# Kernel optimization log

Hardware: AMD Instinct MI355X
Metric: run time of the kernel (lower is better)

The kernel has to match this reference:

```python
import jax, jax.numpy as jnp
import numpy as np

N = 100000

def _gcn_layer(x, W, b, row, col, n):
    # x: [N, Fin] -> lin -> [N, Fout]
    h = x @ W + b
    # degree over row (includes self loops), dtype follows x
    deg = jnp.zeros((n,), dtype=h.dtype).at[row].add(jnp.ones_like(row, dtype=h.dtype))
    dis = deg ** -0.5
    norm = dis[row] * dis[col]                      # [E]
    msg = norm[:, None] * h[row]                    # gather + scale: [E, Fout]
    return jax.ops.segment_sum(msg, col, num_segments=n)  # scatter-add at targets


def setup_inputs() -> dict:
    key = jax.random.key(0)
    ks = jax.random.split(key, 10)
    x = jax.random.normal(ks[0], (N, 32), dtype=jnp.float32)
    feat = jax.random.normal(ks[1], (N, 32), dtype=jnp.float32)
    edge_index = jax.random.randint(ks[2], (2, 1600000), 0, N, dtype=jnp.int64)
    # params (torch Linear stored as [in, out] here; y = x @ W + b)
    def lin(k, fin, fout):
        s = 1.0 / np.sqrt(fin)
        kw, kb = jax.random.split(k)
        W = jax.random.uniform(kw, (fin, fout), minval=-s, maxval=s, dtype=jnp.float32)
        b = jax.random.uniform(kb, (fout,), minval=-s, maxval=s, dtype=jnp.float32)
        return W, b
    W1, b1 = lin(ks[3], 64, 64)
    W2, b2 = lin(ks[4], 64, 64)
    Wfc, bfc = lin(ks[5], 64, 64)
    return {"x": x, "feat": feat, "edge_index": edge_index,
            "W1": W1, "b1": b1, "W2": W2, "b2": b2, "Wfc": Wfc, "bfc": bfc}


def reference(x, feat, edge_index, W1, b1, W2, b2, Wfc, bfc):
    n = x.shape[0]
    h = jnp.concatenate([x, feat], axis=-1)          # [N, 64]
    # add self loops once (same augmented edge set used by every layer)
    loops = jnp.arange(n, dtype=edge_index.dtype)
    row = jnp.concatenate([edge_index[0], loops])
    col = jnp.concatenate([edge_index[1], loops])
    h = jax.nn.relu(_gcn_layer(h, W1, b1, row, col, n))
    h = jax.nn.relu(_gcn_layer(h, W2, b2, row, col, n))
    return jax.nn.relu(h @ Wfc + bfc)                # [N, 64]
```

## Files before the change

kernel.cpp:

```cpp
#include <hip/hip_runtime.h>
#include <hip/hip_bf16.h>


#define FDIM 64
#define NPART 8
#define GPB 64
#define NB 256
#define BW 512
#define MAXP 1024
#define GPLIN 1024

typedef __hip_bfloat16 bf16;
typedef short v8s __attribute__((ext_vector_type(8)));
typedef float v4f __attribute__((ext_vector_type(4)));

static __device__ __forceinline__ float ulo2f(unsigned u) {
    union { unsigned x; float f; } v; v.x = u << 16; return v.f;
}
static __device__ __forceinline__ float uhi2f(unsigned u) {
    union { unsigned x; float f; } v; v.x = u & 0xFFFF0000u; return v.f;
}
static __device__ __forceinline__ unsigned f2bu(float f) {
    bf16 b = __float2bfloat16(f);
    return (unsigned)(*(unsigned short*)&b);
}

__global__ void k_h(const int* __restrict__ row, const int* __restrict__ col,
                    unsigned* __restrict__ part, int* __restrict__ M,
                    int E, int n, int psize, int P, int CH) {
    __shared__ unsigned sm[12512];
    int t = threadIdx.x, b = blockIdx.x;
    if (b < NPART * GPB) {
        int p = b >> 6, g = b & 63;
        int base = p * psize;
        int lim = n - base; if (lim > psize) lim = psize;
        for (int i = t; i < lim; i += 256) sm[i] = 0u;
        __syncthreads();
        for (int e = g * 256 + t; e < E; e += GPB * 256) {
            int r = row[e] - base;
            if ((unsigned)r < (unsigned)lim) atomicAdd(&sm[r], 1u);
        }
        __syncthreads();
        unsigned* dst = part + ((size_t)p * GPB + g) * psize;
        for (int i = t; i < lim; i += 256) dst[i] = sm[i];
    } else {
        int cb = b - NPART * GPB;
        int* h = (int*)sm;
        for (int i = t; i < P; i += 256) h[i] = 0;
        __syncthreads();
        int s = cb * CH, e = min(s + CH, E);
        for (int i = s + t; i < e; i += 256)
            atomicAdd(&h[col[i] >> 9], 1);
        __syncthreads();
        for (int p = t; p < P; p += 256) M[p * NB + cb] = h[p];
    }
}

__global__ void k_ds1(const unsigned* __restrict__ part, float* __restrict__ dis,
                      int* __restrict__ M, int* __restrict__ bsum,
                      int n, int psize, int ndis, int P) {
    __shared__ int sc[256];
    int t = threadIdx.x, b = blockIdx.x;
    if (b < ndis) {
        int i = b * 256 + t;
        if (i >= n) return;
        int p = i / psize, loc = i - p * psize;
        const unsigned* src = part + (size_t)p * GPB * psize + loc;
        unsigned s = 0;
        #pragma unroll 8
        for (int g = 0; g < GPB; ++g) s += src[(size_t)g * psize];
        dis[i] = rsqrtf((float)s + 1.0f);
    } else {
        int sb = b - ndis;
        int i = sb * 256 + t;
        int v = M[i];
        sc[t] = v;
        __syncthreads();
        for (int d = 1; d < 256; d <<= 1) {
            int u = (t >= d) ? sc[t - d] : 0;
            __syncthreads(); sc[t] += u; __syncthreads();
        }
        M[i] = sc[t] - v;
        if (t == 255) bsum[sb] = sc[255];
    }
}

__global__ void k_csc(const int* __restrict__ row, const int* __restrict__ col,
                      const int* __restrict__ M, const int* __restrict__ bsum,
                      int* __restrict__ s4, int E, int CH, int P) {
    __shared__ int sc[256];
    __shared__ int bs[256];
    __shared__ int cur[MAXP];
    int t = threadIdx.x, b = blockIdx.x;
    int v = (t < P) ? bsum[t] : 0;
    sc[t] = v;
    __syncthreads();
    for (int d = 1; d < 256; d <<= 1) {
        int u = (t >= d) ? sc[t - d] : 0;
        __syncthreads(); sc[t] += u; __syncthreads();
    }
    bs[t] = sc[t] - v;
    __syncthreads();
    for (int p = t; p < P; p += 256) cur[p] = bs[p] + M[p * NB + b];
    __syncthreads();
    int s = b * CH, e = min(s + CH, E);
    for (int i = s + t; i < e; i += 256) {
        int r = row[i], c = col[i];
        int pos = atomicAdd(&cur[c >> 9], 1);
        s4[pos] = (r << 9) | (c & 511);
    }
}

__global__ __launch_bounds__(256, 4)
void k_fl(const int* __restrict__ s4, const int* __restrict__ M,
          const int* __restrict__ bsum, int* __restrict__ rows4,
          int* __restrict__ off,
          const float* __restrict__ x, const float* __restrict__ feat,
          const float* __restrict__ W, const float* __restrict__ bvec,
          const float* __restrict__ dis, bf16* __restrict__ g1,
          int n, int E, int P) {
    __shared__ int sc[256];
    __shared__ int bs[256];
    __shared__ int hist[BW];
    __shared__ int loff[BW];
    __shared__ int tmp[256];
    __shared__ float sIn[4][FDIM];
    int t = threadIdx.x, b = blockIdx.x;
    if (b < P) {
        int v = (t < P) ? bsum[t] : 0;
        sc[t] = v;
        __syncthreads();
        for (int d = 1; d < 256; d <<= 1) {
            int u = (t >= d) ? sc[t - d] : 0;
            __syncthreads(); sc[t] += u; __syncthreads();
        }
        bs[t] = sc[t] - v;
        __syncthreads();
        int gs = bs[b];
        int ge = gs + bsum[b];
        int c0 = b << 9;
        int lim = n - c0; if (lim > BW) lim = BW;
        hist[2 * t] = 0; hist[2 * t + 1] = 0;
        __syncthreads();
        for (int i = gs + t; i < ge; i += 256)
            atomicAdd(&hist[s4[i] & 511], 1);
        __syncthreads();
        int s0 = hist[2 * t], s1v = hist[2 * t + 1];
        int ps = s0 + s1v;
        tmp[t] = ps;
        __syncthreads();
        for (int d = 1; d < 256; d <<= 1) {
            int u = (t >= d) ? tmp[t - d] : 0;
            __syncthreads(); tmp[t] += u; __syncthreads();
        }
        int ex = tmp[t] - ps;
        loff[2 * t] = ex;
        loff[2 * t + 1] = ex + s0;
        __syncthreads();
        for (int i = t; i < lim; i += 256) off[c0 + i] = gs + loff[i];
        if (b == P - 1 && t == 0) off[n] = E;
        __syncthreads();
        for (int i = gs + t; i < ge; i += 256) {
            int v2 = s4[i];
            int pos = gs + atomicAdd(&loff[v2 & 511], 1);
            rows4[pos] = v2 >> 9;
        }
    } else {
        int local = t >> 6, j = t & 63;
        float Wreg[FDIM];
        #pragma unroll
        for (int k = 0; k < FDIM; ++k) Wreg[k] = W[k * FDIM + j];
        float bj = bvec[j];
        int gw = (b - P) * 4 + local;
        int nwl = GPLIN * 4;
        for (int w = gw; w < n; w += nwl) {
            sIn[local][j] = (j < 32) ? x[(size_t)w * 32 + j]
                                     : feat[(size_t)w * 32 + (j - 32)];
            __threadfence_block();
            float o = bj;
            #pragma unroll
            for (int k4 = 0; k4 < 16; ++k4) {
                float4 h4 = *(const float4*)&sIn[local][k4 * 4];
                o = fmaf(h4.x, Wreg[4 * k4 + 0], o);
                o = fmaf(h4.y, Wreg[4 * k4 + 1], o);
                o = fmaf(h4.z, Wreg[4 * k4 + 2], o);
                o = fmaf(h4.w, Wreg[4 * k4 + 3], o);
            }
            g1[(size_t)w * FDIM + j] = __float2bfloat16(dis[w] * o);
            __threadfence_block();
        }
    }
}

__global__ __launch_bounds__(256, 8)
void k_gather(const int* __restrict__ rows4, const int* __restrict__ off,
              const float* __restrict__ dis, const bf16* __restrict__ g,
              bf16* __restrict__ a, int n) {
    int t = blockIdx.x * blockDim.x + threadIdx.x;
    int w = t >> 6;
    if (w >= n) return;
    int lane = threadIdx.x & 63;
    int h = lane >> 5;
    int j2 = lane & 31;
    const unsigned* g32 = (const unsigned*)g;
    float acc0 = 0.0f, acc1 = 0.0f;
    int s = off[w], e = off[w + 1];
    for (int k = s; k < e; k += 16) {
        #pragma unroll
        for (int i = 0; i < 8; ++i) {
            int idx = k + 2 * i + h;
            int r = rows4[min(idx, e - 1)];
            unsigned u = g32[(size_t)r * 32 + j2];
            float wg = (idx < e) ? 1.0f : 0.0f;
            acc0 = fmaf(wg, ulo2f(u), acc0);
            acc1 = fmaf(wg, uhi2f(u), acc1);
        }
    }
    acc0 += __shfl_xor(acc0, 32, 64);
    acc1 += __shfl_xor(acc1, 32, 64);
    if (h == 0) {
        unsigned su = g32[(size_t)w * 32 + j2];
        float dv = dis[w];
        float v0 = fmaxf(dv * (acc0 + ulo2f(su)), 0.0f);
        float v1 = fmaxf(dv * (acc1 + uhi2f(su)), 0.0f);
        ((unsigned*)a)[(size_t)w * 32 + j2] = f2bu(v0) | (f2bu(v1) << 16);
    }
}

template <bool FINAL>
__global__ __launch_bounds__(256, 4)
void k_mat(const bf16* __restrict__ A, const float* __restrict__ W,
           const float* __restrict__ bvec, const float* __restrict__ dis,
           void* __restrict__ outp, int n) {
    __shared__ __align__(16) bf16 sWt[FDIM * FDIM];
    int t = threadIdx.x;
    for (int idx = t; idx < FDIM * FDIM; idx += 256) {
        int kk = idx >> 6, nn = idx & 63;
        sWt[nn * FDIM + kk] = __float2bfloat16(W[idx]);
    }
    __syncthreads();
    int wave = t >> 6, lane = t & 63;
    int quad = lane >> 4, l15 = lane & 15;
    v8s bfr[4][2];
    #pragma unroll
    for (int nt = 0; nt < 4; ++nt) {
        #pragma unroll
        for (int kf = 0; kf < 2; ++kf)
            bfr[nt][kf] = *(const v8s*)&sWt[(nt * 16 + l15) * FDIM + kf * 32 + quad * 8];
    }
    float bj[4];
    #pragma unroll
    for (int nt = 0; nt < 4; ++nt) bj[nt] = bvec[nt * 16 + l15];

    int ntiles = (n + 15) >> 4;
    int step = gridDim.x * 4;
    for (int tile = blockIdx.x * 4 + wave; tile < ntiles; tile += step) {
        int m0 = tile << 4;
        int mA = m0 + l15; if (mA >= n) mA = n - 1;
        v8s af0 = *(const v8s*)&A[(size_t)mA * FDIM + quad * 8];
        v8s af1 = *(const v8s*)&A[(size_t)mA * FDIM + 32 + quad * 8];
        v4f acc[4];
        #pragma unroll
        for (int nt = 0; nt < 4; ++nt) {
            acc[nt] = (v4f){0.f, 0.f, 0.f, 0.f};
            acc[nt] = __builtin_amdgcn_mfma_f32_16x16x32_bf16(af0, bfr[nt][0], acc[nt], 0, 0, 0);
            acc[nt] = __builtin_amdgcn_mfma_f32_16x16x32_bf16(af1, bfr[nt][1], acc[nt], 0, 0, 0);
        }
        #pragma unroll
        for (int r = 0; r < 4; ++r) {
            int node = m0 + quad * 4 + r;
            if (node >= n) continue;
            float dv = FINAL ? 0.0f : dis[node];
            #pragma unroll
            for (int nt = 0; nt < 4; ++nt) {
                int j = nt * 16 + l15;
                float o = acc[nt][r] + bj[nt];
                if (FINAL) ((float*)outp)[(size_t)node * FDIM + j] = fmaxf(o, 0.0f);
                else ((bf16*)outp)[(size_t)node * FDIM + j] = __float2bfloat16(dv * o);
            }
        }
    }
}

extern "C" void kernel_launch(void* const* d_in, const int* in_sizes, int n_in,
                              void* d_out, int out_size, void* d_ws, size_t ws_size,
                              hipStream_t stream) {
    const float* x    = (const float*)d_in[0];
    const float* feat = (const float*)d_in[1];
    const int*   ei   = (const int*)d_in[2];
    const float* W1   = (const float*)d_in[3];
    const float* b1   = (const float*)d_in[4];
    const float* W2   = (const float*)d_in[5];
    const float* b2   = (const float*)d_in[6];
    const float* Wfc  = (const float*)d_in[7];
    const float* bfc  = (const float*)d_in[8];
    float* out = (float*)d_out;

    const int n = in_sizes[0] / 32;
    const int E = in_sizes[2] / 2;
    const int* row = ei;
    const int* col = ei + E;

    const int psize = (n + NPART - 1) / NPART;
    const int P  = (n + BW - 1) / BW;
    const int CH = (E + NB - 1) / NB;
    const int total = P * NB;
    const int ndis = (n + 255) / 256;

    int*   off  = (int*)d_ws;
    float* dis  = (float*)(off + (size_t)n + 1);
    int*   M    = (int*)(dis + n);
    int*   bsum = M + (size_t)total;
    int*   s4    = bsum + 256;
    int*   rows4 = s4 + E;
    size_t co = (size_t)(rows4 + E - (int*)d_ws);
    co = (co + 3) & ~(size_t)3;
    bf16*  bufA  = (bf16*)((int*)d_ws + co);
    bf16*  bufB  = bufA + (size_t)n * FDIM;
    unsigned* part = (unsigned*)bufA;

    const int B = 256;

    k_h<<<NPART * GPB + NB, B, 0, stream>>>(row, col, part, M, E, n, psize, P, CH);
    k_ds1<<<ndis + P, B, 0, stream>>>(part, dis, M, bsum, n, psize, ndis, P);
    k_csc<<<NB, B, 0, stream>>>(row, col, M, bsum, s4, E, CH, P);
    k_fl<<<P + GPLIN, B, 0, stream>>>(s4, M, bsum, rows4, off,
                                      x, feat, W1, b1, dis, bufA, n, E, P);
    k_gather<<<(n + 3) / 4, B, 0, stream>>>(rows4, off, dis, bufA, bufB, n);
    k_mat<false><<<512, B, 0, stream>>>(bufB, W2, b2, dis, bufA, n);
    k_gather<<<(n + 3) / 4, B, 0, stream>>>(rows4, off, dis, bufA, bufB, n);
    k_mat<true><<<512, B, 0, stream>>>(bufB, Wfc, bfc, dis, out, n);
}
```

Baseline: 298.3 us.

## Replace partitioned LDS degree histogram with global atomics; split gather tail loop

Degree counting previously ran 512 blocks that each scanned an edge stripe into a per-partition LDS histogram, followed by a 64-way reduction in k_ds1. It now zeroes a global degree array with a memset and has 512 blocks do global atomicAdd per edge, and k_ds1 reads that count directly. This removes the redundant edge scans and the partial-sum reduction, but adds random global atomics with contention plus an extra memset launch. The gather kernel also gets an unmasked main loop over full 16-edge chunks and keeps the masked version only for the tail.

```diff
diff --git a/kernel.cpp b/kernel.cpp
--- a/kernel.cpp
+++ b/kernel.cpp
@@ -3,9 +3,8 @@
 
 
 #define FDIM 64
-#define NPART 8
-#define GPB 64
 #define NB 256
+#define NDEG 512
 #define BW 512
 #define MAXP 1024
 #define GPLIN 1024
@@ -26,50 +25,33 @@
 }
 
 __global__ void k_h(const int* __restrict__ row, const int* __restrict__ col,
-                    unsigned* __restrict__ part, int* __restrict__ M,
-                    int E, int n, int psize, int P, int CH) {
-    __shared__ unsigned sm[12512];
+                    unsigned* __restrict__ deg, int* __restrict__ M,
+                    int E, int n, int P, int CH) {
+    __shared__ int h[MAXP];
     int t = threadIdx.x, b = blockIdx.x;
-    if (b < NPART * GPB) {
-        int p = b >> 6, g = b & 63;
-        int base = p * psize;
-        int lim = n - base; if (lim > psize) lim = psize;
-        for (int i = t; i < lim; i += 256) sm[i] = 0u;
-        __syncthreads();
-        for (int e = g * 256 + t; e < E; e += GPB * 256) {
-            int r = row[e] - base;
-            if ((unsigned)r < (unsigned)lim) atomicAdd(&sm[r], 1u);
-        }
-        __syncthreads();
-        unsigned* dst = part + ((size_t)p * GPB + g) * psize;
-        for (int i = t; i < lim; i += 256) dst[i] = sm[i];
-    } else {
-        int cb = b - NPART * GPB;
-        int* h = (int*)sm;
+    if (b < NB) {
         for (int i = t; i < P; i += 256) h[i] = 0;
         __syncthreads();
-        int s = cb * CH, e = min(s + CH, E);
+        int s = b * CH, e = min(s + CH, E);
         for (int i = s + t; i < e; i += 256)
             atomicAdd(&h[col[i] >> 9], 1);
         __syncthreads();
-        for (int p = t; p < P; p += 256) M[p * NB + cb] = h[p];
-    }
-}
-
-__global__ void k_ds1(const unsigned* __restrict__ part, float* __restrict__ dis,
+        for (int p = t; p < P; p += 256) M[p * NB + b] = h[p];
+    } else {
+        int db = b - NB;
+        for (int i = db * 256 + t; i < E; i += NDEG * 256)
+            atomicAdd(&deg[row[i]], 1u);
+    }
+}
+
+__global__ void k_ds1(const unsigned* __restrict__ deg, float* __restrict__ dis,
                       int* __restrict__ M, int* __restrict__ bsum,
-                      int n, int psize, int ndis, int P) {
+                      int n, int ndis, int P) {
     __shared__ int sc[256];
     int t = threadIdx.x, b = blockIdx.x;
     if (b < ndis) {
         int i = b * 256 + t;
-        if (i >= n) return;
-        int p = i / psize, loc = i - p * psize;
-        const unsigned* src = part + (size_t)p * GPB * psize + loc;
-        unsigned s = 0;
-        #pragma unroll 8
-        for (int g = 0; g < GPB; ++g) s += src[(size_t)g * psize];
-        dis[i] = rsqrtf((float)s + 1.0f);
+        if (i < n) dis[i] = rsqrtf((float)deg[i] + 1.0f);
     } else {
         int sb = b - ndis;
         int i = sb * 256 + t;
@@ -205,7 +187,17 @@
     const unsigned* g32 = (const unsigned*)g;
     float acc0 = 0.0f, acc1 = 0.0f;
     int s = off[w], e = off[w + 1];
-    for (int k = s; k < e; k += 16) {
+    int k = s;
+    for (; k + 16 <= e; k += 16) {
+        #pragma unroll
+        for (int i = 0; i < 8; ++i) {
+            int r = rows4[k + 2 * i + h];
+            unsigned u = g32[(size_t)r * 32 + j2];
+            acc0 += ulo2f(u);
+            acc1 += uhi2f(u);
+        }
+    }
+    if (k < e) {
         #pragma unroll
         for (int i = 0; i < 8; ++i) {
             int idx = k + 2 * i + h;
@@ -301,7 +293,6 @@
     const int* row = ei;
     const int* col = ei + E;
 
-    const int psize = (n + NPART - 1) / NPART;
     const int P  = (n + BW - 1) / BW;
     const int CH = (E + NB - 1) / NB;
     const int total = P * NB;
@@ -317,12 +308,13 @@
     co = (co + 3) & ~(size_t)3;
     bf16*  bufA  = (bf16*)((int*)d_ws + co);
     bf16*  bufB  = bufA + (size_t)n * FDIM;
-    unsigned* part = (unsigned*)bufA;
+    unsigned* deg = (unsigned*)bufA;
 
     const int B = 256;
 
-    k_h<<<NPART * GPB + NB, B, 0, stream>>>(row, col, part, M, E, n, psize, P, CH);
-    k_ds1<<<ndis + P, B, 0, stream>>>(part, dis, M, bsum, n, psize, ndis, P);
+    hipMemsetAsync(deg, 0, (size_t)n * sizeof(unsigned), stream);
+    k_h<<<NB + NDEG, B, 0, stream>>>(row, col, deg, M, E, n, P, CH);
+    k_ds1<<<ndis + P, B, 0, stream>>>(deg, dis, M, bsum, n, ndis, P);
     k_csc<<<NB, B, 0, stream>>>(row, col, M, bsum, s4, E, CH, P);
     k_fl<<<P + GPLIN, B, 0, stream>>>(s4, M, bsum, rows4, off,
                                       x, feat, W1, b1, dis, bufA, n, E, P);
```

After: 328.2 us. 1.1x slower.

## Pack degree histogram counters into bytes and halve partition passes

Applied to the files above, without the earlier changes.

The degree histogram now packs four 8-bit counters into each 32-bit LDS word, so each partition covers four times as many nodes in the same shared memory. This lets the partition count drop from 8 to 4, halving the number of full passes over the row array and shrinking the partial-histogram buffer. The reduction kernel unpacks the four bytes and writes four inverse-sqrt degrees per thread. The risk is byte overflow if any node gets more than 255 edges within one block's slice. Random inputs stay far below that, but skewed graphs would give wrong degrees.

```diff
diff --git a/kernel.cpp b/kernel.cpp
--- a/kernel.cpp
+++ b/kernel.cpp
@@ -3,7 +3,7 @@
 
 
 #define FDIM 64
-#define NPART 8
+#define NPART 4
 #define GPB 64
 #define NB 256
 #define BW 512
@@ -27,22 +27,25 @@
 
 __global__ void k_h(const int* __restrict__ row, const int* __restrict__ col,
                     unsigned* __restrict__ part, int* __restrict__ M,
-                    int E, int n, int psize, int P, int CH) {
-    __shared__ unsigned sm[12512];
+                    int E, int n, int psize, int psize4, int P, int CH) {
+    __shared__ unsigned sm[6256];
     int t = threadIdx.x, b = blockIdx.x;
     if (b < NPART * GPB) {
         int p = b >> 6, g = b & 63;
         int base = p * psize;
         int lim = n - base; if (lim > psize) lim = psize;
-        for (int i = t; i < lim; i += 256) sm[i] = 0u;
-        __syncthreads();
+        int lim4 = (lim + 3) >> 2;
+        for (int i = t; i < lim4; i += 256) sm[i] = 0u;
+        __syncthreads();
+        #pragma unroll 4
         for (int e = g * 256 + t; e < E; e += GPB * 256) {
             int r = row[e] - base;
-            if ((unsigned)r < (unsigned)lim) atomicAdd(&sm[r], 1u);
-        }
-        __syncthreads();
-        unsigned* dst = part + ((size_t)p * GPB + g) * psize;
-        for (int i = t; i < lim; i += 256) dst[i] = sm[i];
+            if ((unsigned)r < (unsigned)lim)
+                atomicAdd(&sm[r >> 2], 1u << ((r & 3) * 8));
+        }
+        __syncthreads();
+        unsigned* dst = part + ((size_t)p * GPB + g) * psize4;
+        for (int i = t; i < lim4; i += 256) dst[i] = sm[i];
     } else {
         int cb = b - NPART * GPB;
         int* h = (int*)sm;
@@ -58,20 +61,28 @@
 
 __global__ void k_ds1(const unsigned* __restrict__ part, float* __restrict__ dis,
                       int* __restrict__ M, int* __restrict__ bsum,
-                      int n, int psize, int ndis, int P) {
+                      int n, int psize4, int ndis4, int P) {
     __shared__ int sc[256];
     int t = threadIdx.x, b = blockIdx.x;
-    if (b < ndis) {
-        int i = b * 256 + t;
+    if (b < ndis4) {
+        int i4 = b * 256 + t;
+        int i = i4 * 4;
         if (i >= n) return;
-        int p = i / psize, loc = i - p * psize;
-        const unsigned* src = part + (size_t)p * GPB * psize + loc;
-        unsigned s = 0;
+        int p = i4 / psize4, loc = i4 - p * psize4;
+        const unsigned* src = part + (size_t)p * GPB * psize4 + loc;
+        unsigned s0 = 0, s1 = 0, s2 = 0, s3 = 0;
         #pragma unroll 8
-        for (int g = 0; g < GPB; ++g) s += src[(size_t)g * psize];
-        dis[i] = rsqrtf((float)s + 1.0f);
+        for (int g = 0; g < GPB; ++g) {
+            unsigned u = src[(size_t)g * psize4];
+            s0 += u & 255u; s1 += (u >> 8) & 255u;
+            s2 += (u >> 16) & 255u; s3 += u >> 24;
+        }
+        dis[i] = rsqrtf((float)s0 + 1.0f);
+        if (i + 1 < n) dis[i + 1] = rsqrtf((float)s1 + 1.0f);
+        if (i + 2 < n) dis[i + 2] = rsqrtf((float)s2 + 1.0f);
+        if (i + 3 < n) dis[i + 3] = rsqrtf((float)s3 + 1.0f);
     } else {
-        int sb = b - ndis;
+        int sb = b - ndis4;
         int i = sb * 256 + t;
         int v = M[i];
         sc[t] = v;
@@ -301,11 +312,12 @@
     const int* row = ei;
     const int* col = ei + E;
 
-    const int psize = (n + NPART - 1) / NPART;
+    const int psize = (((n + NPART - 1) / NPART) + 3) & ~3;
+    const int psize4 = psize >> 2;
     const int P  = (n + BW - 1) / BW;
     const int CH = (E + NB - 1) / NB;
     const int total = P * NB;
-    const int ndis = (n + 255) / 256;
+    const int ndis4 = (((n + 3) / 4) + 255) / 256;
 
     int*   off  = (int*)d_ws;
     float* dis  = (float*)(off + (size_t)n + 1);
@@ -321,8 +333,8 @@
 
     const int B = 256;
 
-    k_h<<<NPART * GPB + NB, B, 0, stream>>>(row, col, part, M, E, n, psize, P, CH);
-    k_ds1<<<ndis + P, B, 0, stream>>>(part, dis, M, bsum, n, psize, ndis, P);
+    k_h<<<NPART * GPB + NB, B, 0, stream>>>(row, col, part, M, E, n, psize, psize4, P, CH);
+    k_ds1<<<ndis4 + P, B, 0, stream>>>(part, dis, M, bsum, n, psize4, ndis4, P);
     k_csc<<<NB, B, 0, stream>>>(row, col, M, bsum, s4, E, CH, P);
     k_fl<<<P + GPLIN, B, 0, stream>>>(s4, M, bsum, rows4, off,
                                       x, feat, W1, b1, dis, bufA, n, E, P);
```

Result: faster. 287.2 us (-3.7%).
